# Kernel tuning notes

Hardware: AMD Instinct MI355X
Metric: run time of the kernel (lower is better)

The kernel has to match this reference:

```python
import jax, jax.numpy as jnp
import numpy as np

B, K, D, DICT, C = 2048, 32, 768, 24576, 64


def setup_inputs() -> dict:
    key = jax.random.key(0)
    ks = jax.random.split(key, 9)
    up_vals = jax.random.uniform(ks[0], (B, K), dtype=jnp.float32)
    up_decoder_w = jax.random.normal(ks[1], (D, DICT), dtype=jnp.float32) * 0.02
    down_encoder_w = jax.random.normal(ks[2], (DICT, D), dtype=jnp.float32) * 0.02
    up_encoder_w = jax.random.normal(ks[3], (DICT, D), dtype=jnp.float32) * 0.02
    b_dec = jax.random.normal(ks[4], (D,), dtype=jnp.float32) * 0.02
    up_indices = jax.random.randint(ks[5], (B, K), 0, DICT)
    down_indices = jax.random.randint(ks[6], (B, K), 0, DICT)
    conn = jax.random.randint(ks[7], (DICT, C), 0, DICT)
    drop = jax.random.uniform(ks[8], (DICT, C)) < 0.1
    connections = jnp.where(drop, -1, conn)
    return {
        "up_vals": up_vals,
        "up_decoder_w": up_decoder_w,
        "down_encoder_w": down_encoder_w,
        "up_encoder_w": up_encoder_w,
        "b_dec": b_dec,
        "up_indices": up_indices,
        "down_indices": down_indices,
        "connections": connections,
    }


def reference(up_vals, up_decoder_w, down_encoder_w, up_encoder_w, b_dec,
              up_indices, down_indices, connections):
    # allowed upstream features per active downstream feature: [B, k_down, C]
    allowed = connections[down_indices]
    valid = allowed != -1
    # match[b,i,c,j] = allowed[b,i,c] == up_indices[b,j] (and slot valid)
    match = (allowed[..., None] == up_indices[:, None, None, :]) & valid[..., None]
    # multiplicity of each (down i, up j) pair across the C slots: [B, k_down, k_up]
    mult = match.sum(axis=2).astype(up_vals.dtype)
    # gather active decoder/encoder vectors
    act_up = up_decoder_w.T[up_indices]          # [B, k_up, D]
    act_down = down_encoder_w[down_indices]      # [B, k_down, D]
    # virtual weights between active down and up features
    vw = jnp.einsum('bid,bjd->bij', act_down, act_up)  # [B, k_down, k_up]
    contributions = jnp.einsum('bij,bij->bi', vw, mult * up_vals[:, None, :])
    # bias contribution (note: indexed by up_indices, broadcast add as in source)
    b_dec_contrib = up_encoder_w @ b_dec         # [DICT]
    return contributions + b_dec_contrib[up_indices]
```

## Files before the change

kernel.cpp:

```cpp
#include <hip/hip_runtime.h>

#define B_    2048
#define K_    32
#define D_    768
#define DICT_ 24576
#define C_    64

__global__ void transpose_kernel(const float* __restrict__ A, float* __restrict__ T) {
    __shared__ float tile[32][33];
    int x = blockIdx.x * 32 + threadIdx.x;
    #pragma unroll
    for (int k = 0; k < 4; ++k) {
        int y = blockIdx.y * 32 + threadIdx.y + k * 8;
        tile[threadIdx.y + k * 8][threadIdx.x] = A[(size_t)y * DICT_ + x];
    }
    __syncthreads();
    int tx = blockIdx.y * 32 + threadIdx.x;
    #pragma unroll
    for (int k = 0; k < 4; ++k) {
        int ty = blockIdx.x * 32 + threadIdx.y + k * 8;
        T[(size_t)ty * D_ + tx] = tile[threadIdx.x][threadIdx.y + k * 8];
    }
}

__global__ void bdc_kernel(const float* __restrict__ up_enc,
                           const float* __restrict__ b_dec,
                           float* __restrict__ bdc) {
    int wave = threadIdx.x >> 6;
    int lane = threadIdx.x & 63;
    int row  = blockIdx.x * 4 + wave;
    const float4* rp = (const float4*)(up_enc + (size_t)row * D_);
    const float4* bp = (const float4*)b_dec;
    float acc = 0.f;
    #pragma unroll
    for (int i = 0; i < 3; ++i) {
        float4 a = rp[lane + 64 * i];
        float4 b = bp[lane + 64 * i];
        acc += a.x * b.x + a.y * b.y + a.z * b.z + a.w * b.w;
    }
    #pragma unroll
    for (int off = 32; off; off >>= 1) acc += __shfl_xor(acc, off);
    if (lane == 0) bdc[row] = acc;
}

__global__ void main_kernel(const float* __restrict__ up_vals,
                            const float* __restrict__ up_dec,
                            const float* __restrict__ down_enc,
                            const float* __restrict__ up_enc,
                            const float* __restrict__ b_dec,
                            const int*   __restrict__ up_idx,
                            const int*   __restrict__ down_idx,
                            const int*   __restrict__ conn,
                            const float* __restrict__ T,
                            const float* __restrict__ bdc,
                            float* __restrict__ out) {
    int wave = threadIdx.x >> 6;
    int lane = threadIdx.x & 63;
    int item = blockIdx.x * 4 + wave;
    int b    = item >> 5;

    int di = down_idx[item];
    int allowed = conn[(size_t)di * C_ + lane];
    bool valid = allowed >= 0;
    int   myup  = up_idx[b * K_ + (lane & 31)];
    float myval = up_vals[b * K_ + (lane & 31)];

    const float* drow = down_enc + (size_t)di * D_;
    float acc = 0.f;

    #pragma unroll 1
    for (int j = 0; j < K_; ++j) {
        int tgt = __shfl(myup, j);
        unsigned long long m = __ballot(valid && (allowed == tgt));
        if (m != 0) {
            float w = (float)__popcll(m) * __shfl(myval, j);
            float partial = 0.f;
            if (T) {
                const float4* cp = (const float4*)(T + (size_t)tgt * D_);
                const float4* dp = (const float4*)drow;
                #pragma unroll
                for (int ii = 0; ii < 3; ++ii) {
                    float4 c = cp[lane + 64 * ii];
                    float4 d = dp[lane + 64 * ii];
                    partial += c.x * d.x + c.y * d.y + c.z * d.z + c.w * d.w;
                }
            } else {
                for (int d = lane; d < D_; d += 64)
                    partial += drow[d] * up_dec[(size_t)d * DICT_ + tgt];
            }
            acc += w * partial;
        }
    }

    if (!bdc) {
        int ui = up_idx[item];
        const float4* rp = (const float4*)(up_enc + (size_t)ui * D_);
        const float4* bp = (const float4*)b_dec;
        #pragma unroll
        for (int ii = 0; ii < 3; ++ii) {
            float4 a  = rp[lane + 64 * ii];
            float4 bb = bp[lane + 64 * ii];
            acc += a.x * bb.x + a.y * bb.y + a.z * bb.z + a.w * bb.w;
        }
    }

    #pragma unroll
    for (int off = 32; off; off >>= 1) acc += __shfl_xor(acc, off);
    if (lane == 0) {
        float bias = bdc ? bdc[up_idx[item]] : 0.f;
        out[item] = acc + bias;
    }
}

extern "C" void kernel_launch(void* const* d_in, const int* in_sizes, int n_in,
                              void* d_out, int out_size, void* d_ws, size_t ws_size,
                              hipStream_t stream) {
    (void)in_sizes; (void)n_in; (void)out_size;
    const float* up_vals  = (const float*)d_in[0];
    const float* up_dec   = (const float*)d_in[1];
    const float* down_enc = (const float*)d_in[2];
    const float* up_enc   = (const float*)d_in[3];
    const float* b_dec    = (const float*)d_in[4];
    const int*   up_idx   = (const int*)d_in[5];
    const int*   down_idx = (const int*)d_in[6];
    const int*   conn     = (const int*)d_in[7];
    float* out = (float*)d_out;

    size_t bdc_bytes = (size_t)DICT_ * sizeof(float);
    size_t T_bytes   = (size_t)DICT_ * D_ * sizeof(float);
    float* bdc = (ws_size >= bdc_bytes) ? (float*)d_ws : nullptr;
    float* T   = (ws_size >= bdc_bytes + T_bytes) ? (float*)d_ws + DICT_ : nullptr;

    if (T) {
        dim3 grid(DICT_ / 32, D_ / 32);
        transpose_kernel<<<grid, dim3(32, 8), 0, stream>>>(up_dec, T);
    }
    if (bdc) {
        bdc_kernel<<<DICT_ / 4, 256, 0, stream>>>(up_enc, b_dec, bdc);
    }
    main_kernel<<<(B_ * K_) / 4, 256, 0, stream>>>(up_vals, up_dec, down_enc, up_enc,
                                                   b_dec, up_idx, down_idx, conn,
                                                   T, bdc, out);
}
```

Before: 265.4 us.

## Drop up_dec transpose; gather strided columns only for sparse matches

Removes the full transpose of the decoder matrix into workspace and instead reads the needed column directly with strided loads, only when a match exists. Match detection is hoisted into a per-lane bitmask built with readlane, followed by an early wave-level skip. This trades a large dense memory pass for uncoalesced gathers that occur only on the rare matching pairs.

```diff
diff --git a/kernel.cpp b/kernel.cpp
--- a/kernel.cpp
+++ b/kernel.cpp
@@ -5,23 +5,6 @@
 #define D_    768
 #define DICT_ 24576
 #define C_    64
-
-__global__ void transpose_kernel(const float* __restrict__ A, float* __restrict__ T) {
-    __shared__ float tile[32][33];
-    int x = blockIdx.x * 32 + threadIdx.x;
-    #pragma unroll
-    for (int k = 0; k < 4; ++k) {
-        int y = blockIdx.y * 32 + threadIdx.y + k * 8;
-        tile[threadIdx.y + k * 8][threadIdx.x] = A[(size_t)y * DICT_ + x];
-    }
-    __syncthreads();
-    int tx = blockIdx.y * 32 + threadIdx.x;
-    #pragma unroll
-    for (int k = 0; k < 4; ++k) {
-        int ty = blockIdx.x * 32 + threadIdx.y + k * 8;
-        T[(size_t)ty * D_ + tx] = tile[threadIdx.x][threadIdx.y + k * 8];
-    }
-}
 
 __global__ void bdc_kernel(const float* __restrict__ up_enc,
                            const float* __restrict__ b_dec,
@@ -51,7 +34,6 @@
                             const int*   __restrict__ up_idx,
                             const int*   __restrict__ down_idx,
                             const int*   __restrict__ conn,
-                            const float* __restrict__ T,
                             const float* __restrict__ bdc,
                             float* __restrict__ out) {
     int wave = threadIdx.x >> 6;
@@ -65,30 +47,31 @@
     int   myup  = up_idx[b * K_ + (lane & 31)];
     float myval = up_vals[b * K_ + (lane & 31)];
 
-    const float* drow = down_enc + (size_t)di * D_;
+    unsigned jm = 0u;
+    #pragma unroll
+    for (int j = 0; j < K_; ++j) {
+        int tgt = __builtin_amdgcn_readlane(myup, j);
+        jm |= (valid && (allowed == tgt)) ? (1u << j) : 0u;
+    }
+
     float acc = 0.f;
-
-    #pragma unroll 1
-    for (int j = 0; j < K_; ++j) {
-        int tgt = __shfl(myup, j);
-        unsigned long long m = __ballot(valid && (allowed == tgt));
-        if (m != 0) {
-            float w = (float)__popcll(m) * __shfl(myval, j);
-            float partial = 0.f;
-            if (T) {
-                const float4* cp = (const float4*)(T + (size_t)tgt * D_);
-                const float4* dp = (const float4*)drow;
+    if (__ballot(jm != 0u)) {
+        const float* drow = down_enc + (size_t)di * D_;
+        #pragma unroll 1
+        for (int j = 0; j < K_; ++j) {
+            unsigned long long m = __ballot((jm >> j) & 1u);
+            if (m != 0) {
+                float w   = (float)__popcll(m) * __shfl(myval, j);
+                int   tgt = __shfl(myup, j);
+                const float* colp = up_dec + tgt;
+                float partial = 0.f;
                 #pragma unroll
-                for (int ii = 0; ii < 3; ++ii) {
-                    float4 c = cp[lane + 64 * ii];
-                    float4 d = dp[lane + 64 * ii];
-                    partial += c.x * d.x + c.y * d.y + c.z * d.z + c.w * d.w;
+                for (int ii = 0; ii < 12; ++ii) {
+                    int d = lane + 64 * ii;
+                    partial += drow[d] * colp[(size_t)d * DICT_];
                 }
-            } else {
-                for (int d = lane; d < D_; d += 64)
-                    partial += drow[d] * up_dec[(size_t)d * DICT_ + tgt];
+                acc += w * partial;
             }
-            acc += w * partial;
         }
     }
 
@@ -127,18 +110,12 @@
     float* out = (float*)d_out;
 
     size_t bdc_bytes = (size_t)DICT_ * sizeof(float);
-    size_t T_bytes   = (size_t)DICT_ * D_ * sizeof(float);
     float* bdc = (ws_size >= bdc_bytes) ? (float*)d_ws : nullptr;
-    float* T   = (ws_size >= bdc_bytes + T_bytes) ? (float*)d_ws + DICT_ : nullptr;
 
-    if (T) {
-        dim3 grid(DICT_ / 32, D_ / 32);
-        transpose_kernel<<<grid, dim3(32, 8), 0, stream>>>(up_dec, T);
-    }
     if (bdc) {
         bdc_kernel<<<DICT_ / 4, 256, 0, stream>>>(up_enc, b_dec, bdc);
     }
-    main_kernel<<<(B_ * K_) / 4, 256, 0, stream>>>(up_vals, up_dec, down_enc, up_enc,
-                                                   b_dec, up_idx, down_idx, conn,
-                                                   T, bdc, out);
+    main_kernel<<<(B_ * K_) / 4, 256, 0, stream>>>(up_vals, up_dec, down_enc,
+                                                   up_enc, b_dec, up_idx,
+                                                   down_idx, conn, bdc, out);
 }
```

New measurement: 265.9 us. About the same (+0.2%).
